# Performance work log

Hardware: AMD Instinct MI355X
Metric: run time of the kernel (lower is better)

## Reference

```python
import jax, jax.numpy as jnp
import numpy as np

L, B, N, C = 6, 8, 300, 20
H, W = 28, 28
GT_H, GT_W = 448, 448


def _pair_similarity(rm_b):
    # rm_b: (N, H, W). Pairwise (IoU + Dice)/2 between thresholded (>0.7) masks.
    T = (rm_b.reshape(N, H * W) > 0.7).astype(jnp.float32)
    inter = T @ T.T                                  # (N, N)
    s = T.sum(axis=1)
    union = s[:, None] + s[None, :] - inter
    tot = s[:, None] + s[None, :]
    iou = jnp.where(union == 0, 1.0, inter / jnp.where(union == 0, 1.0, union))
    dice = jnp.where(tot == 0, 1.0, 2.0 * inter / jnp.where(tot == 0, 1.0, tot))
    return 0.5 * (iou + dice)


def _cluster(S_b, cls_sc):
    # NMS-style greedy transitive expansion from the top-scoring candidate.
    # Equivalent to the torch while-loop: fin_{k+1} = {j in cand : max_{i in fin_k} S[i,j] > 0.5}
    cand = cls_sc > 0.01
    has_cand = jnp.any(cand)
    adj = S_b > 0.5                                   # (N, N) similarity graph
    seed = jnp.argmax(jnp.where(cand, cls_sc, -jnp.inf))
    fin0 = cand & adj[seed]                           # seed always included (S[seed,seed]=1)

    def cond(st):
        return st[1]

    def body(st):
        fin = st[0]
        new = cand & jnp.any(adj & fin[:, None], axis=0)
        return (new, jnp.any(new != fin))

    fin = jax.lax.while_loop(cond, body, (fin0, jnp.array(True)))[0]
    fallback = jnp.arange(N) == jnp.argmax(cls_sc)    # no candidate above 0.01 -> argmax only
    return jnp.where(has_cand, fin, fallback)


def _safe_log(x):
    # matches torch BCELoss log clamping (log clamped at -100)
    return jnp.where(x > 0, jnp.log(jnp.maximum(x, 1e-38)), -100.0)


def _forward(score_map, score, label, gt):
    # per-query CAMs, relu'd and max-normalized
    rm = jax.nn.relu(jnp.mean(score_map, axis=0).reshape(B, N, H, W))
    mx = jnp.max(rm, axis=(-2, -1), keepdims=True)
    rm = rm / (mx + 1e-6)

    S = jax.lax.stop_gradient(jax.vmap(_pair_similarity)(rm))   # (B, N, N)
    sc = jax.lax.stop_gradient(score)                            # used only in comparisons

    def pair_loss(rm_b, S_b, sc_b, gt_b, c):
        fin = _cluster(S_b, sc_b[:, c]).astype(jnp.float32)      # (N,)
        # mean over selected masks commutes with bilinear resize (linear op)
        mean_map = jnp.einsum('n,nhw->hw', fin, rm_b) / jnp.sum(fin)
        pred = jax.image.resize(mean_map, (GT_H, GT_W), method='linear')  # align_corners=False
        y = (gt_b == c + 1).astype(jnp.float32)
        return -jnp.mean(y * _safe_log(pred) + (1.0 - y) * _safe_log(1.0 - pred))

    cls = jnp.arange(C)
    per_b = jax.vmap(lambda rm_b, S_b, sc_b, gt_b:
                     jax.vmap(lambda c: pair_loss(rm_b, S_b, sc_b, gt_b, c))(cls))
    losses = per_b(rm, S, sc, gt)                                # (B, C)
    act = (label != 0).astype(jnp.float32)
    return jnp.sum(losses * act) / jnp.sum(act)


def setup_inputs() -> dict:
    key = jax.random.key(0)
    k1, k2, k3, k4 = jax.random.split(key, 4)
    return {
        'score_map': jax.random.normal(k1, (L, B, N, H * W), dtype=jnp.float32),
        'score': jax.random.uniform(k2, (B, N, C), dtype=jnp.float32),
        'label': jax.random.randint(k3, (B, C), 0, 2).astype(jnp.int32),
        'gt': jax.random.randint(k4, (B, GT_H, GT_W), 0, C + 1).astype(jnp.int32),
    }


def reference(score_map, score, label, gt):
    return _forward(score_map, score, label, gt)
```

## Files before the change

kernel.cpp:

```cpp
#include <hip/hip_runtime.h>
#include <math.h>

#define LNUM 6
#define BNUM 8
#define NNUM 300
#define CNUM 20
#define HW   784
#define GH   448
#define NW   13
#define AW   5
#define RTILE 16
#define NTILE 28

__device__ float              g_rm [BNUM*NNUM*HW];
__device__ unsigned long long g_T  [BNUM*NNUM*NW];
__device__ int                g_s  [BNUM*NNUM];
__device__ unsigned long long g_adj[BNUM*NNUM*AW];
__device__ unsigned long long g_fin[BNUM*CNUM*AW];
__device__ int                g_cnt[BNUM*CNUM];
__device__ float              g_mm [BNUM*CNUM*HW];
__device__ double             g_part[BNUM*CNUM*NTILE];

__global__ void k_rm(const float* __restrict__ sm) {
    int bn  = blockIdx.x;
    int tid = threadIdx.x;
    __shared__ float wmax[4];
    __shared__ int   scount;
    if (tid == 0) scount = 0;
    const size_t lstride = (size_t)BNUM * NNUM * HW;
    const float* base = sm + (size_t)bn * HW;
    float v[4];
    float lm = 0.0f;
    #pragma unroll
    for (int k = 0; k < 4; ++k) {
        int p = k * 256 + tid;
        float a = 0.0f;
        if (p < HW) {
            #pragma unroll
            for (int l = 0; l < LNUM; ++l) a += base[(size_t)l * lstride + p];
            a = __fdiv_rn(a, 6.0f);
            a = fmaxf(a, 0.0f);
        }
        v[k] = a;
        lm = fmaxf(lm, a);
    }
    #pragma unroll
    for (int off = 32; off; off >>= 1) lm = fmaxf(lm, __shfl_xor(lm, off));
    if ((tid & 63) == 0) wmax[tid >> 6] = lm;
    __syncthreads();
    float mx = fmaxf(fmaxf(wmax[0], wmax[1]), fmaxf(wmax[2], wmax[3]));
    float d = mx + 1e-6f;
    #pragma unroll
    for (int k = 0; k < 4; ++k) {
        int p = k * 256 + tid;
        float nv = __fdiv_rn(v[k], d);
        if (p < HW) g_rm[(size_t)bn * HW + p] = nv;
        bool pr = (p < HW) && (nv > 0.7f);
        unsigned long long ball = __ballot(pr);
        int word = k * 4 + (tid >> 6);
        if ((tid & 63) == 0 && word < NW) {
            g_T[(size_t)bn * NW + word] = ball;
            atomicAdd(&scount, __popcll(ball));
        }
    }
    __syncthreads();
    if (tid == 0) g_s[bn] = scount;
}

__global__ void k_adj() {
    int blk = blockIdx.x;
    int b = blk / NNUM;
    int tid = threadIdx.x;
    __shared__ unsigned long long Ti[NW];
    __shared__ int si_sh;
    if (tid < NW)  Ti[tid] = g_T[(size_t)blk * NW + tid];
    if (tid == NW) si_sh = g_s[blk];
    __syncthreads();
    bool a = false;
    int j = tid;
    if (j < NNUM) {
        const unsigned long long* Tj = &g_T[((size_t)b * NNUM + j) * NW];
        int inter = 0;
        #pragma unroll
        for (int w = 0; w < NW; ++w) inter += __popcll(Ti[w] & Tj[w]);
        int si = si_sh, sj = g_s[b * NNUM + j];
        int uni = si + sj - inter, tot = si + sj;
        float iou  = (uni == 0) ? 1.0f : __fdiv_rn((float)inter, (float)uni);
        float dice = (tot == 0) ? 1.0f : __fdiv_rn(2.0f * (float)inter, (float)tot);
        a = (0.5f * (iou + dice)) > 0.5f;
    }
    unsigned long long ball = __ballot(a);
    if ((tid & 63) == 0) g_adj[(size_t)blk * AW + (tid >> 6)] = ball;
}

__global__ void k_cluster(const float* __restrict__ score, const int* __restrict__ label) {
    int blk = blockIdx.x;
    if (label[blk] == 0) return;
    int b = blk / CNUM, c = blk - b * CNUM;
    int lane = threadIdx.x;
    __shared__ unsigned long long adj_sh[NNUM][AW];
    __shared__ unsigned long long cand[AW], fin[AW], nw[AW];
    for (int idx = lane; idx < NNUM * AW; idx += 64)
        ((unsigned long long*)adj_sh)[idx] = g_adj[(size_t)b * NNUM * AW + idx];
    float bv = -INFINITY; int bi = NNUM;
    float bva = -INFINITY; int bia = NNUM;
    for (int k = 0; k < AW; ++k) {
        int j = k * 64 + lane;
        bool cb = false;
        if (j < NNUM) {
            float sc = score[((size_t)b * NNUM + j) * CNUM + c];
            if (sc > bva) { bva = sc; bia = j; }
            cb = sc > 0.01f;
            if (cb && sc > bv) { bv = sc; bi = j; }
        }
        unsigned long long ball = __ballot(cb);
        if (lane == 0) cand[k] = ball;
    }
    #pragma unroll
    for (int off = 1; off < 64; off <<= 1) {
        float ov = __shfl_xor(bv, off);  int oi = __shfl_xor(bi, off);
        if (ov > bv || (ov == bv && oi < bi)) { bv = ov; bi = oi; }
        float ova = __shfl_xor(bva, off); int oia = __shfl_xor(bia, off);
        if (ova > bva || (ova == bva && oia < bia)) { bva = ova; bia = oia; }
    }
    __syncthreads();
    bool has = (cand[0] | cand[1] | cand[2] | cand[3] | cand[4]) != 0ULL;
    if (!has) {
        if (lane < AW) g_fin[(size_t)blk * AW + lane] = ((bia >> 6) == lane) ? (1ULL << (bia & 63)) : 0ULL;
        if (lane == 0) g_cnt[blk] = 1;
        return;
    }
    int seed = bi;
    if (lane < AW) fin[lane] = cand[lane] & adj_sh[seed][lane];
    __syncthreads();
    for (int it = 0; it < NNUM + 2; ++it) {
        for (int k = 0; k < AW; ++k) {
            int j = k * 64 + lane;
            bool nb = false;
            if (j < NNUM && ((cand[k] >> lane) & 1ULL)) {
                unsigned long long o = (adj_sh[j][0] & fin[0]) | (adj_sh[j][1] & fin[1]) |
                                       (adj_sh[j][2] & fin[2]) | (adj_sh[j][3] & fin[3]) |
                                       (adj_sh[j][4] & fin[4]);
                nb = (o != 0ULL);
            }
            unsigned long long ball = __ballot(nb);
            if (lane == 0) nw[k] = ball;
        }
        __syncthreads();
        bool ch = (lane < AW) && (nw[lane] != fin[lane]);
        unsigned long long chb = __ballot(ch);
        if (lane < AW) fin[lane] = nw[lane];
        __syncthreads();
        if (chb == 0) break;
    }
    if (lane < AW) g_fin[(size_t)blk * AW + lane] = fin[lane];
    if (lane == 0) {
        int cs = 0;
        for (int w = 0; w < AW; ++w) cs += __popcll(fin[w]);
        g_cnt[blk] = cs;
    }
}

__global__ void k_meanmap(const int* __restrict__ label) {
    int blk = blockIdx.x;
    if (label[blk] == 0) return;
    int b = blk / CNUM;
    int tid = threadIdx.x;
    __shared__ unsigned long long f[AW];
    __shared__ float cf;
    if (tid < AW)  f[tid] = g_fin[(size_t)blk * AW + tid];
    if (tid == AW) cf = (float)g_cnt[blk];
    __syncthreads();
    float a0 = 0.f, a1 = 0.f, a2 = 0.f, a3 = 0.f;
    for (int w = 0; w < AW; ++w) {
        unsigned long long word = f[w];
        while (word) {
            int j = w * 64 + (__ffsll((unsigned long long)word) - 1);
            word &= word - 1;
            const float* r = &g_rm[((size_t)b * NNUM + j) * HW];
            a0 += r[tid];
            a1 += r[256 + tid];
            a2 += r[512 + tid];
            if (tid < 16) a3 += r[768 + tid];
        }
    }
    float cc = cf;
    g_mm[(size_t)blk * HW + tid]       = __fdiv_rn(a0, cc);
    g_mm[(size_t)blk * HW + 256 + tid] = __fdiv_rn(a1, cc);
    g_mm[(size_t)blk * HW + 512 + tid] = __fdiv_rn(a2, cc);
    if (tid < 16) g_mm[(size_t)blk * HW + 768 + tid] = __fdiv_rn(a3, cc);
}

__global__ void k_bce(const int* __restrict__ gt, const int* __restrict__ label) {
    int blk = blockIdx.x;
    int bc = blk / NTILE, tile = blk - bc * NTILE;
    if (label[bc] == 0) return;
    int b = bc / CNUM, c = bc - b * CNUM;
    int tid = threadIdx.x;
    __shared__ float m[HW];
    __shared__ float rowY[RTILE * 28];
    for (int p = tid; p < HW; p += 256) m[p] = g_mm[(size_t)bc * HW + p];
    __syncthreads();
    int row0 = tile * RTILE;
    for (int idx = tid; idx < RTILE * 28; idx += 256) {
        int r = idx / 28, x = idx - r * 28;
        int oy = row0 + r;
        float iy = fmaf((float)oy, 0.0625f, -0.46875f);
        float y0f = floorf(iy);
        float wy = iy - y0f;
        int y0 = (int)y0f;
        if (y0 < 0) { y0 = 0; wy = 0.0f; } else if (y0 > 26) { y0 = 26; wy = 1.0f; }
        float lo = m[y0 * 28 + x], hi = m[y0 * 28 + 28 + x];
        rowY[idx] = lo + wy * (hi - lo);
    }
    __syncthreads();
    double acc = 0.0;
    int cp1 = c + 1;
    const int* gtb = gt + (size_t)b * GH * GH + (size_t)row0 * GH;
    #pragma unroll
    for (int pass = 0; pass < 2; ++pass) {
        int ox = tid + pass * 256;
        if (ox >= GH) break;
        float ixc = fmaf((float)ox, 0.0625f, -0.46875f);
        float x0f = floorf(ixc);
        float wx = ixc - x0f;
        int x0 = (int)x0f;
        if (x0 < 0) { x0 = 0; wx = 0.0f; } else if (x0 > 26) { x0 = 26; wx = 1.0f; }
        #pragma unroll 4
        for (int r = 0; r < RTILE; ++r) {
            float rY0 = rowY[r * 28 + x0];
            float rY1 = rowY[r * 28 + x0 + 1];
            float pred = rY0 + wx * (rY1 - rY0);
            int g = gtb[r * GH + ox];
            float xv = (g == cp1) ? pred : 1.0f - pred;
            float lg = __logf(fmaxf(xv, 1.175494351e-38f));
            acc += (double)((xv > 0.0f) ? lg : -100.0f);
        }
    }
    #pragma unroll
    for (int off = 32; off; off >>= 1) acc += __shfl_xor(acc, off);
    __shared__ double wsum[4];
    if ((tid & 63) == 0) wsum[tid >> 6] = acc;
    __syncthreads();
    if (tid == 0)
        g_part[blk] = -(wsum[0] + wsum[1] + wsum[2] + wsum[3]) * (1.0 / (448.0 * 448.0));
}

__global__ void k_final(const int* __restrict__ label, float* __restrict__ out) {
    int tid = threadIdx.x;
    double s = 0.0;
    for (int i = tid; i < BNUM * CNUM * NTILE; i += 256)
        if (label[i / NTILE] != 0) s += g_part[i];
    #pragma unroll
    for (int off = 32; off; off >>= 1) s += __shfl_xor(s, off);
    __shared__ double wsum[4];
    if ((tid & 63) == 0) wsum[tid >> 6] = s;
    __syncthreads();
    if (tid == 0) {
        int sa = 0;
        for (int i = 0; i < BNUM * CNUM; ++i) sa += (label[i] != 0) ? 1 : 0;
        out[0] = (float)((wsum[0] + wsum[1] + wsum[2] + wsum[3]) / (double)sa);
    }
}

extern "C" void kernel_launch(void* const* d_in, const int* in_sizes, int n_in,
                              void* d_out, int out_size, void* d_ws, size_t ws_size,
                              hipStream_t stream) {
    const float* sm    = (const float*)d_in[0];
    const float* score = (const float*)d_in[1];
    const int*   label = (const int*)d_in[2];
    const int*   gt    = (const int*)d_in[3];
    float* out = (float*)d_out;

    hipLaunchKernelGGL(k_rm,      dim3(BNUM * NNUM),          dim3(256), 0, stream, sm);
    hipLaunchKernelGGL(k_adj,     dim3(BNUM * NNUM),          dim3(320), 0, stream);
    hipLaunchKernelGGL(k_cluster, dim3(BNUM * CNUM),          dim3(64),  0, stream, score, label);
    hipLaunchKernelGGL(k_meanmap, dim3(BNUM * CNUM),          dim3(256), 0, stream, label);
    hipLaunchKernelGGL(k_bce,     dim3(BNUM * CNUM * NTILE),  dim3(256), 0, stream, gt, label);
    hipLaunchKernelGGL(k_final,   dim3(1),                    dim3(256), 0, stream, label, out);
}
```

Baseline: 62.33 us.

## Vectorize loads, fuse cluster with mean-map, and restructure BCE upsample per segment

k_rm now reads score_map as float4 with one thread per four pixels, and the bit-mask word count is padded from 13 to 16. The clustering and mean-map kernels are merged into one 256-thread kernel so the fin bitset stays in shared memory and one launch and a global round-trip are removed. k_bce runs 448 threads, each handling one 16-pixel horizontal segment between two source columns: it reads gt as int4 and computes the interpolation weights in closed form. Edge segments reuse a single log pair weighted by a count of matches. The fused kernel keeps three of four waves idle while the clustering iterations run, and the new BCE indexing depends on the fixed 16x upsampling geometry.

```diff
diff --git a/kernel.cpp b/kernel.cpp
--- a/kernel.cpp
+++ b/kernel.cpp
@@ -6,8 +6,9 @@
 #define NNUM 300
 #define CNUM 20
 #define HW   784
+#define HW4  196
 #define GH   448
-#define NW   13
+#define NW   16
 #define AW   5
 #define RTILE 16
 #define NTILE 28
@@ -16,50 +17,50 @@
 __device__ unsigned long long g_T  [BNUM*NNUM*NW];
 __device__ int                g_s  [BNUM*NNUM];
 __device__ unsigned long long g_adj[BNUM*NNUM*AW];
-__device__ unsigned long long g_fin[BNUM*CNUM*AW];
-__device__ int                g_cnt[BNUM*CNUM];
 __device__ float              g_mm [BNUM*CNUM*HW];
 __device__ double             g_part[BNUM*CNUM*NTILE];
 
 __global__ void k_rm(const float* __restrict__ sm) {
     int bn  = blockIdx.x;
     int tid = threadIdx.x;
+    int lane = tid & 63, wid = tid >> 6;
     __shared__ float wmax[4];
     __shared__ int   scount;
     if (tid == 0) scount = 0;
-    const size_t lstride = (size_t)BNUM * NNUM * HW;
-    const float* base = sm + (size_t)bn * HW;
-    float v[4];
-    float lm = 0.0f;
-    #pragma unroll
-    for (int k = 0; k < 4; ++k) {
-        int p = k * 256 + tid;
-        float a = 0.0f;
-        if (p < HW) {
-            #pragma unroll
-            for (int l = 0; l < LNUM; ++l) a += base[(size_t)l * lstride + p];
-            a = __fdiv_rn(a, 6.0f);
-            a = fmaxf(a, 0.0f);
-        }
-        v[k] = a;
-        lm = fmaxf(lm, a);
-    }
+    const size_t lstr4 = (size_t)BNUM * NNUM * HW4;
+    const float4* base = (const float4*)sm + (size_t)bn * HW4;
+    bool act = tid < HW4;
+    float4 v = {0.f, 0.f, 0.f, 0.f};
+    if (act) {
+        float4 a = {0.f, 0.f, 0.f, 0.f};
+        #pragma unroll
+        for (int l = 0; l < LNUM; ++l) {
+            float4 x = base[(size_t)l * lstr4 + tid];
+            a.x += x.x; a.y += x.y; a.z += x.z; a.w += x.w;
+        }
+        v.x = fmaxf(__fdiv_rn(a.x, 6.0f), 0.0f);
+        v.y = fmaxf(__fdiv_rn(a.y, 6.0f), 0.0f);
+        v.z = fmaxf(__fdiv_rn(a.z, 6.0f), 0.0f);
+        v.w = fmaxf(__fdiv_rn(a.w, 6.0f), 0.0f);
+    }
+    float lm = fmaxf(fmaxf(v.x, v.y), fmaxf(v.z, v.w));
     #pragma unroll
     for (int off = 32; off; off >>= 1) lm = fmaxf(lm, __shfl_xor(lm, off));
-    if ((tid & 63) == 0) wmax[tid >> 6] = lm;
+    if (lane == 0) wmax[wid] = lm;
     __syncthreads();
     float mx = fmaxf(fmaxf(wmax[0], wmax[1]), fmaxf(wmax[2], wmax[3]));
     float d = mx + 1e-6f;
+    float4 nv;
+    nv.x = __fdiv_rn(v.x, d); nv.y = __fdiv_rn(v.y, d);
+    nv.z = __fdiv_rn(v.z, d); nv.w = __fdiv_rn(v.w, d);
+    if (act) ((float4*)g_rm)[(size_t)bn * HW4 + tid] = nv;
+    float c[4] = {nv.x, nv.y, nv.z, nv.w};
     #pragma unroll
     for (int k = 0; k < 4; ++k) {
-        int p = k * 256 + tid;
-        float nv = __fdiv_rn(v[k], d);
-        if (p < HW) g_rm[(size_t)bn * HW + p] = nv;
-        bool pr = (p < HW) && (nv > 0.7f);
+        bool pr = act && (c[k] > 0.7f);
         unsigned long long ball = __ballot(pr);
-        int word = k * 4 + (tid >> 6);
-        if ((tid & 63) == 0 && word < NW) {
-            g_T[(size_t)bn * NW + word] = ball;
+        if (lane == 0) {
+            g_T[(size_t)bn * NW + k * 4 + wid] = ball;
             atomicAdd(&scount, __popcll(ball));
         }
     }
@@ -93,102 +94,98 @@
     if ((tid & 63) == 0) g_adj[(size_t)blk * AW + (tid >> 6)] = ball;
 }
 
-__global__ void k_cluster(const float* __restrict__ score, const int* __restrict__ label) {
+__global__ void k_cm(const float* __restrict__ score, const int* __restrict__ label) {
     int blk = blockIdx.x;
     if (label[blk] == 0) return;
     int b = blk / CNUM, c = blk - b * CNUM;
-    int lane = threadIdx.x;
+    int tid = threadIdx.x;
+    int lane = tid & 63, wid = tid >> 6;
     __shared__ unsigned long long adj_sh[NNUM][AW];
-    __shared__ unsigned long long cand[AW], fin[AW], nw[AW];
-    for (int idx = lane; idx < NNUM * AW; idx += 64)
+    __shared__ unsigned long long cand[AW], fin[AW], nwv[AW];
+    __shared__ int sh_has, sh_go;
+    __shared__ float sh_cf;
+    for (int idx = tid; idx < NNUM * AW; idx += 256)
         ((unsigned long long*)adj_sh)[idx] = g_adj[(size_t)b * NNUM * AW + idx];
-    float bv = -INFINITY; int bi = NNUM;
-    float bva = -INFINITY; int bia = NNUM;
-    for (int k = 0; k < AW; ++k) {
-        int j = k * 64 + lane;
-        bool cb = false;
-        if (j < NNUM) {
-            float sc = score[((size_t)b * NNUM + j) * CNUM + c];
-            if (sc > bva) { bva = sc; bia = j; }
-            cb = sc > 0.01f;
-            if (cb && sc > bv) { bv = sc; bi = j; }
-        }
-        unsigned long long ball = __ballot(cb);
-        if (lane == 0) cand[k] = ball;
-    }
-    #pragma unroll
-    for (int off = 1; off < 64; off <<= 1) {
-        float ov = __shfl_xor(bv, off);  int oi = __shfl_xor(bi, off);
-        if (ov > bv || (ov == bv && oi < bi)) { bv = ov; bi = oi; }
-        float ova = __shfl_xor(bva, off); int oia = __shfl_xor(bia, off);
-        if (ova > bva || (ova == bva && oia < bia)) { bva = ova; bia = oia; }
-    }
-    __syncthreads();
-    bool has = (cand[0] | cand[1] | cand[2] | cand[3] | cand[4]) != 0ULL;
-    if (!has) {
-        if (lane < AW) g_fin[(size_t)blk * AW + lane] = ((bia >> 6) == lane) ? (1ULL << (bia & 63)) : 0ULL;
-        if (lane == 0) g_cnt[blk] = 1;
-        return;
-    }
-    int seed = bi;
-    if (lane < AW) fin[lane] = cand[lane] & adj_sh[seed][lane];
-    __syncthreads();
-    for (int it = 0; it < NNUM + 2; ++it) {
+    if (wid == 0) {
+        float bv = -INFINITY; int bi = NNUM;
+        float bva = -INFINITY; int bia = NNUM;
         for (int k = 0; k < AW; ++k) {
             int j = k * 64 + lane;
-            bool nb = false;
-            if (j < NNUM && ((cand[k] >> lane) & 1ULL)) {
-                unsigned long long o = (adj_sh[j][0] & fin[0]) | (adj_sh[j][1] & fin[1]) |
-                                       (adj_sh[j][2] & fin[2]) | (adj_sh[j][3] & fin[3]) |
-                                       (adj_sh[j][4] & fin[4]);
-                nb = (o != 0ULL);
-            }
-            unsigned long long ball = __ballot(nb);
-            if (lane == 0) nw[k] = ball;
-        }
-        __syncthreads();
-        bool ch = (lane < AW) && (nw[lane] != fin[lane]);
-        unsigned long long chb = __ballot(ch);
-        if (lane < AW) fin[lane] = nw[lane];
-        __syncthreads();
-        if (chb == 0) break;
-    }
-    if (lane < AW) g_fin[(size_t)blk * AW + lane] = fin[lane];
-    if (lane == 0) {
+            bool cb = false;
+            if (j < NNUM) {
+                float sc = score[((size_t)b * NNUM + j) * CNUM + c];
+                if (sc > bva) { bva = sc; bia = j; }
+                cb = sc > 0.01f;
+                if (cb && sc > bv) { bv = sc; bi = j; }
+            }
+            unsigned long long ball = __ballot(cb);
+            if (lane == 0) cand[k] = ball;
+        }
+        #pragma unroll
+        for (int off = 1; off < 64; off <<= 1) {
+            float ov = __shfl_xor(bv, off);  int oi = __shfl_xor(bi, off);
+            if (ov > bv || (ov == bv && oi < bi)) { bv = ov; bi = oi; }
+            float ova = __shfl_xor(bva, off); int oia = __shfl_xor(bia, off);
+            if (ova > bva || (ova == bva && oia < bia)) { bva = ova; bia = oia; }
+        }
+        bool has = (cand[0] | cand[1] | cand[2] | cand[3] | cand[4]) != 0ULL;
+        if (lane == 0) sh_has = has ? 1 : 0;
+        if (has) {
+            if (lane < AW) fin[lane] = cand[lane] & adj_sh[bi][lane];
+        } else {
+            if (lane < AW) fin[lane] = ((bia >> 6) == lane) ? (1ULL << (bia & 63)) : 0ULL;
+        }
+    }
+    __syncthreads();
+    if (sh_has) {
+        for (int it = 0; it < NNUM + 2; ++it) {
+            if (wid == 0) {
+                for (int k = 0; k < AW; ++k) {
+                    int j = k * 64 + lane;
+                    bool nb = false;
+                    if (j < NNUM && ((cand[k] >> lane) & 1ULL)) {
+                        unsigned long long o = (adj_sh[j][0] & fin[0]) | (adj_sh[j][1] & fin[1]) |
+                                               (adj_sh[j][2] & fin[2]) | (adj_sh[j][3] & fin[3]) |
+                                               (adj_sh[j][4] & fin[4]);
+                        nb = (o != 0ULL);
+                    }
+                    unsigned long long ball = __ballot(nb);
+                    if (lane == 0) nwv[k] = ball;
+                }
+                bool ch = (lane < AW) && (nwv[lane] != fin[lane]);
+                unsigned long long chb = __ballot(ch);
+                if (lane == 0) sh_go = (chb != 0ULL) ? 1 : 0;
+                if (lane < AW) fin[lane] = nwv[lane];
+            }
+            __syncthreads();
+            int go = sh_go;
+            __syncthreads();
+            if (!go) break;
+        }
+    }
+    if (tid == 0) {
         int cs = 0;
         for (int w = 0; w < AW; ++w) cs += __popcll(fin[w]);
-        g_cnt[blk] = cs;
-    }
-}
-
-__global__ void k_meanmap(const int* __restrict__ label) {
-    int blk = blockIdx.x;
-    if (label[blk] == 0) return;
-    int b = blk / CNUM;
-    int tid = threadIdx.x;
-    __shared__ unsigned long long f[AW];
-    __shared__ float cf;
-    if (tid < AW)  f[tid] = g_fin[(size_t)blk * AW + tid];
-    if (tid == AW) cf = (float)g_cnt[blk];
-    __syncthreads();
-    float a0 = 0.f, a1 = 0.f, a2 = 0.f, a3 = 0.f;
-    for (int w = 0; w < AW; ++w) {
-        unsigned long long word = f[w];
-        while (word) {
-            int j = w * 64 + (__ffsll((unsigned long long)word) - 1);
-            word &= word - 1;
-            const float* r = &g_rm[((size_t)b * NNUM + j) * HW];
-            a0 += r[tid];
-            a1 += r[256 + tid];
-            a2 += r[512 + tid];
-            if (tid < 16) a3 += r[768 + tid];
-        }
-    }
-    float cc = cf;
-    g_mm[(size_t)blk * HW + tid]       = __fdiv_rn(a0, cc);
-    g_mm[(size_t)blk * HW + 256 + tid] = __fdiv_rn(a1, cc);
-    g_mm[(size_t)blk * HW + 512 + tid] = __fdiv_rn(a2, cc);
-    if (tid < 16) g_mm[(size_t)blk * HW + 768 + tid] = __fdiv_rn(a3, cc);
+        sh_cf = (float)cs;
+    }
+    __syncthreads();
+    if (tid < HW4) {
+        float4 a = {0.f, 0.f, 0.f, 0.f};
+        for (int w = 0; w < AW; ++w) {
+            unsigned long long word = fin[w];
+            while (word) {
+                int j = w * 64 + (__ffsll(word) - 1);
+                word &= word - 1;
+                float4 r = ((const float4*)g_rm)[((size_t)b * NNUM + j) * HW4 + tid];
+                a.x += r.x; a.y += r.y; a.z += r.z; a.w += r.w;
+            }
+        }
+        float cc = sh_cf;
+        float4 o;
+        o.x = __fdiv_rn(a.x, cc); o.y = __fdiv_rn(a.y, cc);
+        o.z = __fdiv_rn(a.z, cc); o.w = __fdiv_rn(a.w, cc);
+        ((float4*)g_mm)[(size_t)blk * HW4 + tid] = o;
+    }
 }
 
 __global__ void k_bce(const int* __restrict__ gt, const int* __restrict__ label) {
@@ -199,11 +196,12 @@
     int tid = threadIdx.x;
     __shared__ float m[HW];
     __shared__ float rowY[RTILE * 28];
-    for (int p = tid; p < HW; p += 256) m[p] = g_mm[(size_t)bc * HW + p];
+    __shared__ double wsum[7];
+    if (tid < HW4) ((float4*)m)[tid] = ((const float4*)g_mm)[(size_t)bc * HW4 + tid];
     __syncthreads();
     int row0 = tile * RTILE;
-    for (int idx = tid; idx < RTILE * 28; idx += 256) {
-        int r = idx / 28, x = idx - r * 28;
+    {
+        int r = tid / 28, x = tid - r * 28;
         int oy = row0 + r;
         float iy = fmaf((float)oy, 0.0625f, -0.46875f);
         float y0f = floorf(iy);
@@ -211,39 +209,55 @@
         int y0 = (int)y0f;
         if (y0 < 0) { y0 = 0; wy = 0.0f; } else if (y0 > 26) { y0 = 26; wy = 1.0f; }
         float lo = m[y0 * 28 + x], hi = m[y0 * 28 + 28 + x];
-        rowY[idx] = lo + wy * (hi - lo);
-    }
-    __syncthreads();
+        rowY[tid] = lo + wy * (hi - lo);
+    }
+    __syncthreads();
+    int r = tid / 28, j = tid - r * 28;
+    const int* gr = gt + ((size_t)b * GH + row0 + r) * GH;
     double acc = 0.0;
     int cp1 = c + 1;
-    const int* gtb = gt + (size_t)b * GH * GH + (size_t)row0 * GH;
-    #pragma unroll
-    for (int pass = 0; pass < 2; ++pass) {
-        int ox = tid + pass * 256;
-        if (ox >= GH) break;
-        float ixc = fmaf((float)ox, 0.0625f, -0.46875f);
-        float x0f = floorf(ixc);
-        float wx = ixc - x0f;
-        int x0 = (int)x0f;
-        if (x0 < 0) { x0 = 0; wx = 0.0f; } else if (x0 > 26) { x0 = 26; wx = 1.0f; }
-        #pragma unroll 4
-        for (int r = 0; r < RTILE; ++r) {
-            float rY0 = rowY[r * 28 + x0];
-            float rY1 = rowY[r * 28 + x0 + 1];
-            float pred = rY0 + wx * (rY1 - rY0);
-            int g = gtb[r * GH + ox];
-            float xv = (g == cp1) ? pred : 1.0f - pred;
-            float lg = __logf(fmaxf(xv, 1.175494351e-38f));
-            acc += (double)((xv > 0.0f) ? lg : -100.0f);
+    if (j < 27) {
+        float rY0 = rowY[r * 28 + j], rY1 = rowY[r * 28 + j + 1];
+        float sl = rY1 - rY0;
+        const int4* gp = (const int4*)(gr + 16 * j + 8);
+        #pragma unroll
+        for (int q = 0; q < 4; ++q) {
+            int4 g4 = gp[q];
+            #pragma unroll
+            for (int u = 0; u < 4; ++u) {
+                int k = q * 4 + u;
+                int gv = (u == 0) ? g4.x : (u == 1) ? g4.y : (u == 2) ? g4.z : g4.w;
+                float wk = fmaf((float)k, 0.0625f, 0.03125f);
+                float pred = rY0 + wk * sl;
+                float xv = (gv == cp1) ? pred : 1.0f - pred;
+                float lg = __logf(fmaxf(xv, 1.175494351e-38f));
+                acc += (double)((xv > 0.0f) ? lg : -100.0f);
+            }
+        }
+    } else {
+        #pragma unroll
+        for (int side = 0; side < 2; ++side) {
+            float pred = rowY[r * 28 + (side ? 27 : 0)];
+            const int4* gp = (const int4*)(gr + (side ? 440 : 0));
+            int4 a0 = gp[0], a1 = gp[1];
+            int np = (a0.x == cp1) + (a0.y == cp1) + (a0.z == cp1) + (a0.w == cp1)
+                   + (a1.x == cp1) + (a1.y == cp1) + (a1.z == cp1) + (a1.w == cp1);
+            float om = 1.0f - pred;
+            float lgp = (pred > 0.0f) ? __logf(fmaxf(pred, 1.175494351e-38f)) : -100.0f;
+            float lgn = (om   > 0.0f) ? __logf(fmaxf(om,   1.175494351e-38f)) : -100.0f;
+            acc += (double)lgp * (double)np + (double)lgn * (double)(8 - np);
         }
     }
     #pragma unroll
     for (int off = 32; off; off >>= 1) acc += __shfl_xor(acc, off);
-    __shared__ double wsum[4];
     if ((tid & 63) == 0) wsum[tid >> 6] = acc;
     __syncthreads();
-    if (tid == 0)
-        g_part[blk] = -(wsum[0] + wsum[1] + wsum[2] + wsum[3]) * (1.0 / (448.0 * 448.0));
+    if (tid == 0) {
+        double s = 0.0;
+        #pragma unroll
+        for (int w = 0; w < 7; ++w) s += wsum[w];
+        g_part[blk] = -s * (1.0 / (448.0 * 448.0));
+    }
 }
 
 __global__ void k_final(const int* __restrict__ label, float* __restrict__ out) {
@@ -272,10 +286,9 @@
     const int*   gt    = (const int*)d_in[3];
     float* out = (float*)d_out;
 
-    hipLaunchKernelGGL(k_rm,      dim3(BNUM * NNUM),          dim3(256), 0, stream, sm);
-    hipLaunchKernelGGL(k_adj,     dim3(BNUM * NNUM),          dim3(320), 0, stream);
-    hipLaunchKernelGGL(k_cluster, dim3(BNUM * CNUM),          dim3(64),  0, stream, score, label);
-    hipLaunchKernelGGL(k_meanmap, dim3(BNUM * CNUM),          dim3(256), 0, stream, label);
-    hipLaunchKernelGGL(k_bce,     dim3(BNUM * CNUM * NTILE),  dim3(256), 0, stream, gt, label);
-    hipLaunchKernelGGL(k_final,   dim3(1),                    dim3(256), 0, stream, label, out);
-}
+    hipLaunchKernelGGL(k_rm,    dim3(BNUM * NNUM),         dim3(256), 0, stream, sm);
+    hipLaunchKernelGGL(k_adj,   dim3(BNUM * NNUM),         dim3(320), 0, stream);
+    hipLaunchKernelGGL(k_cm,    dim3(BNUM * CNUM),         dim3(256), 0, stream, score, label);
+    hipLaunchKernelGGL(k_bce,   dim3(BNUM * CNUM * NTILE), dim3(448), 0, stream, gt, label);
+    hipLaunchKernelGGL(k_final, dim3(1),                   dim3(256), 0, stream, label, out);
+}
```

New measurement: 63.00 us. Within noise of the previous version (+1.1%).
